# Kernel optimization log

Measured on AMD Instinct MI355X. Metric: run time of the kernel, lower is better.

The kernel has to match this reference:

```python
import jax, jax.numpy as jnp
import numpy as np

B, T, C, H = 2, 2048, 1024, 16
D = C // H  # head dim = 64


def setup_inputs() -> dict:
    key = jax.random.key(0)
    k1, k2, k3 = jax.random.split(key, 3)
    x = jax.random.normal(k1, (B, T, C), dtype=jnp.float32)
    w_attn = jax.random.normal(k2, (C, 3 * C), dtype=jnp.float32) * (1.0 / np.sqrt(C))
    b_attn = jnp.zeros((3 * C,), dtype=jnp.float32)
    w_proj = jax.random.normal(k3, (C, C), dtype=jnp.float32) * (1.0 / np.sqrt(C))
    b_proj = jnp.zeros((C,), dtype=jnp.float32)
    return {"x": x, "w_attn": w_attn, "b_attn": b_attn, "w_proj": w_proj, "b_proj": b_proj}


def reference(x, w_attn, b_attn, w_proj, b_proj):
    Bx, Tx, Cx = x.shape
    qkv = x @ w_attn + b_attn  # [B, T, 3C]
    q, k, v = jnp.split(qkv, 3, axis=-1)
    # [B, H, T, D]
    q = q.reshape(Bx, Tx, H, D).swapaxes(1, 2)
    k = k.reshape(Bx, Tx, H, D).swapaxes(1, 2)
    v = v.reshape(Bx, Tx, H, D).swapaxes(1, 2)
    scale = 1.0 / jnp.sqrt(jnp.float32(D))
    att = jnp.einsum('bhqd,bhkd->bhqk', q, k) * scale  # [B, H, T, T]
    causal = jnp.tril(jnp.ones((Tx, Tx), dtype=bool))
    att = jnp.where(causal[None, None], att, -jnp.inf)
    att = jax.nn.softmax(att, axis=-1)
    y = jnp.einsum('bhqk,bhkd->bhqd', att, v)  # [B, H, T, D]
    y = y.swapaxes(1, 2).reshape(Bx, Tx, Cx)
    return y @ w_proj + b_proj
```

## Files before the change

### kernel.cpp

```cpp
#include <hip/hip_runtime.h>
#include <hip/hip_bf16.h>


typedef __attribute__((ext_vector_type(8))) short short8x;
typedef __attribute__((ext_vector_type(4))) float float4x;
typedef __attribute__((ext_vector_type(4))) unsigned short ushort4x;
typedef __attribute__((ext_vector_type(2))) unsigned int uint2x;

#define MFMA_BF16 __builtin_amdgcn_mfma_f32_16x16x32_bf16

typedef const __attribute__((address_space(1))) void gvoid_t;
typedef __attribute__((address_space(3))) void lvoid_t;
#define GLOAD_LDS16(g, l) __builtin_amdgcn_global_load_lds((gvoid_t*)(g), (lvoid_t*)(l), 16, 0, 0)

__device__ __forceinline__ unsigned short f2b(float f) {
    unsigned int u = __float_as_uint(f);
    u = (u + 0x7FFFu + ((u >> 16) & 1u)) >> 16;
    return (unsigned short)u;
}
__device__ __forceinline__ unsigned int pk2(float a, float b) {
    return __builtin_amdgcn_perm(__float_as_uint(b) + 0x8000u,
                                 __float_as_uint(a) + 0x8000u, 0x07060302u);
}

__device__ __forceinline__ void stage32(const unsigned short* g, size_t rs,
                                        short* ldst, int w0, int lane) {
    const int r8 = lane >> 3;
    const int sc = ((lane & 7) ^ r8) * 8;
#pragma unroll
    for (int q = 0; q < 4; q++) {
        GLOAD_LDS16(g + (size_t)(w0 + q * 8 + r8) * rs + sc,
                    ldst + (w0 + q * 8) * 64);
    }
}

__global__ __launch_bounds__(256) void cast_bf16(const float* __restrict__ in,
                                                 unsigned short* __restrict__ out,
                                                 int n4) {
    int i = blockIdx.x * 256 + threadIdx.x;
    if (i < n4) {
        float4 v = ((const float4*)in)[i];
        ushort4x o = { f2b(v.x), f2b(v.y), f2b(v.z), f2b(v.w) };
        ((ushort4x*)out)[i] = o;
    }
}

__global__ __launch_bounds__(256) void transpose_cast2(const float* __restrict__ wa,
                                                       unsigned short* __restrict__ waT,
                                                       const float* __restrict__ wp,
                                                       unsigned short* __restrict__ wpT) {
    __shared__ float tile[32][33];
    int bx = blockIdx.x;
    const float* in;
    unsigned short* outp;
    int cols;
    if (bx < 96) { in = wa; outp = waT; cols = 3072; }
    else         { in = wp; outp = wpT; cols = 1024; bx -= 96; }
    int cbase = bx * 32;
    int rbase = blockIdx.y * 32;
    int c = cbase + threadIdx.x;
    for (int j = 0; j < 32; j += 8)
        tile[threadIdx.y + j][threadIdx.x] = in[(size_t)(rbase + threadIdx.y + j) * cols + c];
    __syncthreads();
    int rr = rbase + threadIdx.x;
    for (int j = 0; j < 32; j += 8) {
        int cc = cbase + threadIdx.y + j;
        outp[(size_t)cc * 1024 + rr] = f2b(tile[threadIdx.x][threadIdx.y + j]);
    }
}

__global__ __launch_bounds__(256) void gemm_qkv(const unsigned short* __restrict__ A,
                                                const unsigned short* __restrict__ BT,
                                                const float* __restrict__ bias,
                                                unsigned short* __restrict__ QK,
                                                unsigned short* __restrict__ VTg) {
    __shared__ union {
        struct { short A[128 * 64]; short B[128 * 64]; } s;
        short vt[4][64 * 80];
    } lds;

    const int K = 1024;
    const int lane = threadIdx.x & 63;
    const int wave = threadIdx.x >> 6;
    const int quad = lane >> 4;
    const int l16  = lane & 15;
    const int sw   = l16 & 7;

    const int rblk = blockIdx.y * 128;
    const int cblk = blockIdx.x * 128;
    const int wr = wave >> 1, wc = wave & 1;

    float4x acc[4][4] = {};

    const unsigned short* Ag = A  + (size_t)rblk * K;
    const unsigned short* Bg = BT + (size_t)cblk * K;

    for (int kk = 0; kk < K; kk += 64) {
        stage32(Ag + kk, K, lds.s.A, wave * 32, lane);
        stage32(Bg + kk, K, lds.s.B, wave * 32, lane);
        __syncthreads();

#pragma unroll
        for (int kk2 = 0; kk2 < 2; kk2++) {
            short8x a[4], b[4];
#pragma unroll
            for (int i = 0; i < 4; i++)
                a[i] = *(const short8x*)&lds.s.A[(wr * 64 + i * 16 + l16) * 64 +
                                                 ((kk2 * 4 + quad) ^ sw) * 8];
#pragma unroll
            for (int j = 0; j < 4; j++)
                b[j] = *(const short8x*)&lds.s.B[(wc * 64 + j * 16 + l16) * 64 +
                                                 ((kk2 * 4 + quad) ^ sw) * 8];
#pragma unroll
            for (int i = 0; i < 4; i++)
#pragma unroll
                for (int j = 0; j < 4; j++)
                    acc[i][j] = MFMA_BF16(a[i], b[j], acc[i][j], 0, 0, 0);
        }
        __syncthreads();
    }

    const int rbase = rblk + wr * 64;
    const int cbase = cblk + wc * 64;

    if (cbase < 2048) {
        const float QS = 0.18033688f;
#pragma unroll
        for (int i = 0; i < 4; i++) {
#pragma unroll
            for (int j = 0; j < 4; j++) {
                int c = cbase + j * 16 + l16;
                float bv = bias[c];
                float sc = (c < 1024) ? QS : 1.0f;
#pragma unroll
                for (int reg = 0; reg < 4; reg++) {
                    int r = rbase + i * 16 + quad * 4 + reg;
                    QK[(size_t)r * 2048 + c] = f2b((acc[i][j][reg] + bv) * sc);
                }
            }
        }
    } else {
#pragma unroll
        for (int i = 0; i < 4; i++) {
#pragma unroll
            for (int j = 0; j < 4; j++) {
                int c = cbase + j * 16 + l16;
                float bv = bias[c];
                uint2x p = { pk2(acc[i][j][0] + bv, acc[i][j][1] + bv),
                             pk2(acc[i][j][2] + bv, acc[i][j][3] + bv) };
                *(uint2x*)&lds.vt[wave][(j * 16 + l16) * 80 + i * 16 + quad * 4] = p;
            }
        }
        const int h   = (cbase - 2048) >> 6;
        const int hb  = (rbase >> 11) * 16 + h;
        const int tb0 = rbase & 2047;
#pragma unroll
        for (int p = 0; p < 8; p++) {
            int dd   = p * 8 + (lane >> 3);
            int toff = (lane & 7) * 8;
            short8x vv = *(const short8x*)&lds.vt[wave][dd * 80 + toff];
            *(short8x*)&VTg[((size_t)(hb * 64 + dd)) * 2048 + tb0 + toff] = vv;
        }
    }
}

__global__ __launch_bounds__(256) void gemm_proj(const unsigned short* __restrict__ A,
                                                 const unsigned short* __restrict__ BT,
                                                 const float* __restrict__ bias,
                                                 float* __restrict__ out) {
    __shared__ struct { short A[64 * 64]; short B[64 * 64]; } lds;

    const int K = 1024, N = 1024;
    const int lane = threadIdx.x & 63;
    const int wave = threadIdx.x >> 6;
    const int quad = lane >> 4;
    const int l16  = lane & 15;
    const int sw   = l16 & 7;

    const int rblk = blockIdx.y * 64;
    const int cblk = blockIdx.x * 64;

    float4x acc[4] = {};

    const unsigned short* Ag = A  + (size_t)rblk * K;
    const unsigned short* Bg = BT + (size_t)cblk * K;

    for (int kk = 0; kk < K; kk += 64) {
        if (wave < 2) stage32(Ag + kk, K, lds.A, wave * 32, lane);
        else          stage32(Bg + kk, K, lds.B, (wave - 2) * 32, lane);
        __syncthreads();

#pragma unroll
        for (int kk2 = 0; kk2 < 2; kk2++) {
            short8x bfr = *(const short8x*)&lds.B[(wave * 16 + l16) * 64 +
                                                  ((kk2 * 4 + quad) ^ sw) * 8];
#pragma unroll
            for (int i = 0; i < 4; i++) {
                short8x a = *(const short8x*)&lds.A[(i * 16 + l16) * 64 +
                                                    ((kk2 * 4 + quad) ^ sw) * 8];
                acc[i] = MFMA_BF16(a, bfr, acc[i], 0, 0, 0);
            }
        }
        __syncthreads();
    }

    const int c = cblk + wave * 16 + l16;
    const float bv = bias[c];
#pragma unroll
    for (int i = 0; i < 4; i++) {
#pragma unroll
        for (int reg = 0; reg < 4; reg++) {
            int r = rblk + i * 16 + quad * 4 + reg;
            out[(size_t)r * N + c] = acc[i][reg] + bv;
        }
    }
}

__global__ __launch_bounds__(256) void attn_kernel(const unsigned short* __restrict__ QK,
                                                   const unsigned short* __restrict__ VT,
                                                   unsigned short* __restrict__ Y) {
    __shared__ __attribute__((aligned(16))) short Kl[2][64 * 64];
    __shared__ __attribute__((aligned(16))) short Vl[2][64 * 64];
    __shared__ __attribute__((aligned(16))) short Pl[4][16 * 64];

    const int tid  = threadIdx.x;
    const int lane = tid & 63;
    const int wave = tid >> 6;
    const int quad = lane >> 4;
    const int l16  = lane & 15;
    const int sw   = l16 & 7;

    const int bid = blockIdx.x;
    const int v2  = (bid >> 8) & 3;
    const int s2  = ((bid >> 3) & 3) ^ v2;
    const int m3  = (bid >> 5) & 7;
    const int qb  = (s2 == 0) ? m3 : (s2 == 1) ? 15 - m3
                  : (s2 == 2) ? 16 + m3 : 31 - m3;
    const int bh  = (bid & 7) | (v2 << 3);
    const int b = bh >> 4, h = bh & 15;

    const unsigned short* Qp = QK + ((size_t)b * 2048) * 2048 + h * 64;
    const unsigned short* Kp = Qp + 1024;
    const unsigned short* Vp = VT + (size_t)bh * 64 * 2048;

    const int qbase = qb * 64 + wave * 16;
    const int ntb   = qb + 1;

    short8x aq[2];
#pragma unroll
    for (int kk = 0; kk < 2; kk++)
        aq[kk] = *(const short8x*)(Qp + (size_t)(qbase + l16) * 2048 + kk * 32 + quad * 8);

    if (wave < 2) stage32(Kp, 2048, Kl[0], wave * 32, lane);
    else          stage32(Vp, 2048, Vl[0], (wave - 2) * 32, lane);
    __syncthreads();

    float l = 0.f;
    float4x O[4] = {};

    for (int it = 0; it < ntb; it++) {
        const int kb = it * 64;
        const short* Kc = Kl[it & 1];
        const short* Vc = Vl[it & 1];

        if (it + 1 < ntb) {
            const int kb2 = kb + 64;
            if (wave < 2) stage32(Kp + (size_t)kb2 * 2048, 2048, Kl[(it + 1) & 1], wave * 32, lane);
            else          stage32(Vp + kb2, 2048, Vl[(it + 1) & 1], (wave - 2) * 32, lane);
        }

        float4x S[4];
#pragma unroll
        for (int t = 0; t < 4; t++) {
            short8x kf0 = *(const short8x*)&Kc[(t * 16 + l16) * 64 + ((quad) ^ sw) * 8];
            short8x kf1 = *(const short8x*)&Kc[(t * 16 + l16) * 64 + ((4 + quad) ^ sw) * 8];
            S[t] = (float4x){0.f, 0.f, 0.f, 0.f};
            S[t] = MFMA_BF16(kf0, aq[0], S[t], 0, 0, 0);
            S[t] = MFMA_BF16(kf1, aq[1], S[t], 0, 0, 0);
        }

        if (kb + 64 > qbase) {
            int q = qbase + l16;
#pragma unroll
            for (int t = 0; t < 4; t++)
#pragma unroll
                for (int reg = 0; reg < 4; reg++)
                    if (kb + t * 16 + quad * 4 + reg > q) S[t][reg] = -1e38f;
        }

#pragma unroll
        for (int t = 0; t < 4; t++) {
            float e0 = __builtin_amdgcn_exp2f(S[t][0]);
            float e1 = __builtin_amdgcn_exp2f(S[t][1]);
            float e2 = __builtin_amdgcn_exp2f(S[t][2]);
            float e3 = __builtin_amdgcn_exp2f(S[t][3]);
            l += (e0 + e1) + (e2 + e3);
            uint2x p = { pk2(e0, e1), pk2(e2, e3) };
            *(uint2x*)&Pl[wave][l16 * 64 + ((2 * t + (quad >> 1)) ^ sw) * 8 + (quad & 1) * 4] = p;
        }

#pragma unroll
        for (int kc = 0; kc < 2; kc++) {
            short8x bp = *(const short8x*)&Pl[wave][l16 * 64 + ((4 * kc + quad) ^ sw) * 8];
#pragma unroll
            for (int dt = 0; dt < 4; dt++) {
                short8x vf = *(const short8x*)&Vc[(dt * 16 + l16) * 64 + ((kc * 4 + quad) ^ sw) * 8];
                O[dt] = MFMA_BF16(vf, bp, O[dt], 0, 0, 0);
            }
        }
        __syncthreads();
    }

    float lv = l;
    lv += __shfl_xor(lv, 16, 64);
    lv += __shfl_xor(lv, 32, 64);
    float rl = 1.0f / lv;
#pragma unroll
    for (int dt = 0; dt < 4; dt++) {
        uint2x o = { pk2(O[dt][0] * rl, O[dt][1] * rl),
                     pk2(O[dt][2] * rl, O[dt][3] * rl) };
        *(uint2x*)&Pl[wave][l16 * 64 + ((2 * dt + (quad >> 1)) ^ sw) * 8 + (quad & 1) * 4] = o;
    }
    const int t = qbase + l16;
#pragma unroll
    for (int cc = 0; cc < 2; cc++) {
        short8x row = *(const short8x*)&Pl[wave][l16 * 64 + ((2 * quad + cc) ^ sw) * 8];
        *(short8x*)&Y[((size_t)(b * 2048 + t)) * 1024 + h * 64 + (2 * quad + cc) * 8] = row;
    }
}

extern "C" void kernel_launch(void* const* d_in, const int* in_sizes, int n_in,
                              void* d_out, int out_size, void* d_ws, size_t ws_size,
                              hipStream_t stream) {
    const float* x      = (const float*)d_in[0];
    const float* w_attn = (const float*)d_in[1];
    const float* b_attn = (const float*)d_in[2];
    const float* w_proj = (const float*)d_in[3];
    const float* b_proj = (const float*)d_in[4];
    float* out = (float*)d_out;

    char* ws = (char*)d_ws;
    unsigned short* xb  = (unsigned short*)(ws + (size_t)0);
    unsigned short* waT = (unsigned short*)(ws + (size_t)(8  << 20));
    unsigned short* wpT = (unsigned short*)(ws + (size_t)(14 << 20));
    unsigned short* QKb = (unsigned short*)(ws + (size_t)(16 << 20));
    unsigned short* VTb = (unsigned short*)(ws + (size_t)(32 << 20));
    unsigned short* yb  = (unsigned short*)(ws + (size_t)(40 << 20));

    cast_bf16<<<4096, 256, 0, stream>>>(x, xb, 1048576);

    transpose_cast2<<<dim3(128, 32), dim3(32, 8), 0, stream>>>(w_attn, waT, w_proj, wpT);

    gemm_qkv<<<dim3(24, 32), 256, 0, stream>>>(xb, waT, b_attn, QKb, VTb);

    attn_kernel<<<1024, 256, 0, stream>>>(QKb, VTb, yb);

    gemm_proj<<<dim3(16, 64), 256, 0, stream>>>(yb, wpT, b_proj, out);
}
```

Baseline: 182.3 us.

## Merge prep kernels, vectorize QK epilogue stores, widen proj GEMM tile

Folds the x cast and the weight transpose-casts into a single prep launch, which removes one kernel launch. In the QKV GEMM's Q/K blocks, the MFMA operands are swapped so each lane holds four consecutive columns, letting the epilogue write packed bf16 pairs and load the bias as float4 instead of issuing scalar stores. The projection GEMM tile grows from 64x64 to 64x128, halving the grid and reusing each A fragment across two B fragments. The cost is more accumulator registers per thread and fewer blocks in the projection GEMM.

```diff
diff --git a/kernel.cpp b/kernel.cpp
--- a/kernel.cpp
+++ b/kernel.cpp
@@ -34,38 +34,39 @@
     }
 }
 
-__global__ __launch_bounds__(256) void cast_bf16(const float* __restrict__ in,
-                                                 unsigned short* __restrict__ out,
-                                                 int n4) {
-    int i = blockIdx.x * 256 + threadIdx.x;
-    if (i < n4) {
-        float4 v = ((const float4*)in)[i];
+__global__ __launch_bounds__(256) void prep(const float* __restrict__ x,
+                                            unsigned short* __restrict__ xb,
+                                            const float* __restrict__ wa,
+                                            unsigned short* __restrict__ waT,
+                                            const float* __restrict__ wp,
+                                            unsigned short* __restrict__ wpT) {
+    __shared__ float tile[32][33];
+    const int blk = blockIdx.x;
+    if (blk < 4096) {
+        int i = blk * 256 + threadIdx.x;
+        float4 v = ((const float4*)x)[i];
         ushort4x o = { f2b(v.x), f2b(v.y), f2b(v.z), f2b(v.w) };
-        ((ushort4x*)out)[i] = o;
-    }
-}
-
-__global__ __launch_bounds__(256) void transpose_cast2(const float* __restrict__ wa,
-                                                       unsigned short* __restrict__ waT,
-                                                       const float* __restrict__ wp,
-                                                       unsigned short* __restrict__ wpT) {
-    __shared__ float tile[32][33];
-    int bx = blockIdx.x;
+        ((ushort4x*)xb)[i] = o;
+        return;
+    }
+    int idx = blk - 4096;
+    int bx = idx & 127;
+    int by = idx >> 7;
     const float* in;
     unsigned short* outp;
     int cols;
     if (bx < 96) { in = wa; outp = waT; cols = 3072; }
     else         { in = wp; outp = wpT; cols = 1024; bx -= 96; }
-    int cbase = bx * 32;
-    int rbase = blockIdx.y * 32;
-    int c = cbase + threadIdx.x;
+    const int tx = threadIdx.x & 31, ty = threadIdx.x >> 5;
+    const int cbase = bx * 32, rbase = by * 32;
+    int c = cbase + tx;
     for (int j = 0; j < 32; j += 8)
-        tile[threadIdx.y + j][threadIdx.x] = in[(size_t)(rbase + threadIdx.y + j) * cols + c];
+        tile[ty + j][tx] = in[(size_t)(rbase + ty + j) * cols + c];
     __syncthreads();
-    int rr = rbase + threadIdx.x;
+    int rr = rbase + tx;
     for (int j = 0; j < 32; j += 8) {
-        int cc = cbase + threadIdx.y + j;
-        outp[(size_t)cc * 1024 + rr] = f2b(tile[threadIdx.x][threadIdx.y + j]);
+        int cc = cbase + ty + j;
+        outp[(size_t)cc * 1024 + rr] = f2b(tile[tx][ty + j]);
     }
 }
 
@@ -89,6 +90,7 @@
     const int rblk = blockIdx.y * 128;
     const int cblk = blockIdx.x * 128;
     const int wr = wave >> 1, wc = wave & 1;
+    const bool qk = (blockIdx.x < 16);
 
     float4x acc[4][4] = {};
 
@@ -111,11 +113,19 @@
             for (int j = 0; j < 4; j++)
                 b[j] = *(const short8x*)&lds.s.B[(wc * 64 + j * 16 + l16) * 64 +
                                                  ((kk2 * 4 + quad) ^ sw) * 8];
-#pragma unroll
-            for (int i = 0; i < 4; i++)
-#pragma unroll
-                for (int j = 0; j < 4; j++)
-                    acc[i][j] = MFMA_BF16(a[i], b[j], acc[i][j], 0, 0, 0);
+            if (qk) {
+#pragma unroll
+                for (int i = 0; i < 4; i++)
+#pragma unroll
+                    for (int j = 0; j < 4; j++)
+                        acc[i][j] = MFMA_BF16(b[j], a[i], acc[i][j], 0, 0, 0);
+            } else {
+#pragma unroll
+                for (int i = 0; i < 4; i++)
+#pragma unroll
+                    for (int j = 0; j < 4; j++)
+                        acc[i][j] = MFMA_BF16(a[i], b[j], acc[i][j], 0, 0, 0);
+            }
         }
         __syncthreads();
     }
@@ -123,20 +133,18 @@
     const int rbase = rblk + wr * 64;
     const int cbase = cblk + wc * 64;
 
-    if (cbase < 2048) {
-        const float QS = 0.18033688f;
+    if (qk) {
+        const float sc = (blockIdx.x < 8) ? 0.18033688f : 1.0f;
 #pragma unroll
         for (int i = 0; i < 4; i++) {
+            const int r = rbase + i * 16 + l16;
 #pragma unroll
             for (int j = 0; j < 4; j++) {
-                int c = cbase + j * 16 + l16;
-                float bv = bias[c];
-                float sc = (c < 1024) ? QS : 1.0f;
-#pragma unroll
-                for (int reg = 0; reg < 4; reg++) {
-                    int r = rbase + i * 16 + quad * 4 + reg;
-                    QK[(size_t)r * 2048 + c] = f2b((acc[i][j][reg] + bv) * sc);
-                }
+                const int c = cbase + j * 16 + quad * 4;
+                float4 bv = *(const float4*)&bias[c];
+                uint2x p = { pk2((acc[i][j][0] + bv.x) * sc, (acc[i][j][1] + bv.y) * sc),
+                             pk2((acc[i][j][2] + bv.z) * sc, (acc[i][j][3] + bv.w) * sc) };
+                *(uint2x*)&QK[(size_t)r * 2048 + c] = p;
             }
         }
     } else {
@@ -168,7 +176,7 @@
                                                  const unsigned short* __restrict__ BT,
                                                  const float* __restrict__ bias,
                                                  float* __restrict__ out) {
-    __shared__ struct { short A[64 * 64]; short B[64 * 64]; } lds;
+    __shared__ struct { short A[64 * 64]; short B[128 * 64]; } lds;
 
     const int K = 1024, N = 1024;
     const int lane = threadIdx.x & 63;
@@ -178,40 +186,52 @@
     const int sw   = l16 & 7;
 
     const int rblk = blockIdx.y * 64;
-    const int cblk = blockIdx.x * 64;
-
-    float4x acc[4] = {};
+    const int cblk = blockIdx.x * 128;
+
+    float4x acc[4][2] = {};
 
     const unsigned short* Ag = A  + (size_t)rblk * K;
     const unsigned short* Bg = BT + (size_t)cblk * K;
 
     for (int kk = 0; kk < K; kk += 64) {
-        if (wave < 2) stage32(Ag + kk, K, lds.A, wave * 32, lane);
-        else          stage32(Bg + kk, K, lds.B, (wave - 2) * 32, lane);
+        if (wave < 2) {
+            stage32(Ag + kk, K, lds.A, wave * 32, lane);
+        } else {
+            stage32(Bg + kk, K, lds.B, (wave - 2) * 64, lane);
+            stage32(Bg + kk, K, lds.B, (wave - 2) * 64 + 32, lane);
+        }
         __syncthreads();
 
 #pragma unroll
         for (int kk2 = 0; kk2 < 2; kk2++) {
-            short8x bfr = *(const short8x*)&lds.B[(wave * 16 + l16) * 64 +
-                                                  ((kk2 * 4 + quad) ^ sw) * 8];
+            short8x b[2];
+#pragma unroll
+            for (int j = 0; j < 2; j++)
+                b[j] = *(const short8x*)&lds.B[(wave * 32 + j * 16 + l16) * 64 +
+                                               ((kk2 * 4 + quad) ^ sw) * 8];
 #pragma unroll
             for (int i = 0; i < 4; i++) {
                 short8x a = *(const short8x*)&lds.A[(i * 16 + l16) * 64 +
                                                     ((kk2 * 4 + quad) ^ sw) * 8];
-                acc[i] = MFMA_BF16(a, bfr, acc[i], 0, 0, 0);
-            }
-        }
-        __syncthreads();
-    }
-
-    const int c = cblk + wave * 16 + l16;
-    const float bv = bias[c];
-#pragma unroll
-    for (int i = 0; i < 4; i++) {
-#pragma unroll
-        for (int reg = 0; reg < 4; reg++) {
-            int r = rblk + i * 16 + quad * 4 + reg;
-            out[(size_t)r * N + c] = acc[i][reg] + bv;
+#pragma unroll
+                for (int j = 0; j < 2; j++)
+                    acc[i][j] = MFMA_BF16(a, b[j], acc[i][j], 0, 0, 0);
+            }
+        }
+        __syncthreads();
+    }
+
+#pragma unroll
+    for (int j = 0; j < 2; j++) {
+        const int c = cblk + wave * 32 + j * 16 + l16;
+        const float bv = bias[c];
+#pragma unroll
+        for (int i = 0; i < 4; i++) {
+#pragma unroll
+            for (int reg = 0; reg < 4; reg++) {
+                int r = rblk + i * 16 + quad * 4 + reg;
+                out[(size_t)r * N + c] = acc[i][j][reg] + bv;
+            }
         }
     }
 }
@@ -347,13 +367,11 @@
     unsigned short* VTb = (unsigned short*)(ws + (size_t)(32 << 20));
     unsigned short* yb  = (unsigned short*)(ws + (size_t)(40 << 20));
 
-    cast_bf16<<<4096, 256, 0, stream>>>(x, xb, 1048576);
-
-    transpose_cast2<<<dim3(128, 32), dim3(32, 8), 0, stream>>>(w_attn, waT, w_proj, wpT);
+    prep<<<8192, 256, 0, stream>>>(x, xb, w_attn, waT, w_proj, wpT);
 
     gemm_qkv<<<dim3(24, 32), 256, 0, stream>>>(xb, waT, b_attn, QKb, VTb);
 
     attn_kernel<<<1024, 256, 0, stream>>>(QKb, VTb, yb);
 
-    gemm_proj<<<dim3(16, 64), 256, 0, stream>>>(yb, wpT, b_proj, out);
-}
+    gemm_proj<<<dim3(8, 64), 256, 0, stream>>>(yb, wpT, b_proj, out);
+}
```

After: 193.4 us. 6.1% more time.
